# Kernel tuning notes

Hardware: AMD Instinct MI355X
Metric: run time of the kernel (lower is better)

## Reference

```python
import jax, jax.numpy as jnp
import numpy as np

TAU = 0.2
ALPHA = 0.8
EPS = 1e-8  # torch cosine_similarity eps
LAM_POS = 1.5  # generate_lambda()=0.5, +1 for extrapolation
LAM_NEG = 0.5  # interpolation lambda


def _cos_sim_matrix(x):
    # row-normalize with clamped norm (matches F.cosine_similarity eps), then gram matrix
    n = x / jnp.maximum(jnp.linalg.norm(x, axis=1, keepdims=True), EPS)
    return n @ n.T


def setup_inputs() -> dict:
    key = jax.random.key(0)
    N, D = 4096, 512
    emb = jax.random.normal(key, (N, D), dtype=jnp.float32)
    # SimCLR-style symmetric positive pairs: (2k,2k+1) and (2k+1,2k)
    base = np.arange(0, N, 2)
    fwd_pairs = np.stack([base, base + 1], axis=1)
    pairs = np.concatenate([fwd_pairs, fwd_pairs[:, ::-1]], axis=0)  # [N, 2]
    return {"embeddings": emb, "positive_pairs": jnp.asarray(pairs, dtype=jnp.int32)}


def reference(embeddings, positive_pairs):
    # stage == 'train' (quantile-thresholded hard-negative branch)
    N = embeddings.shape[0]
    ar = jnp.arange(N)
    pi, pj = positive_pairs[:, 0], positive_pairs[:, 1]
    # ordered positive mask (symmetric because pairs include both orientations)
    pos_mask = jnp.zeros((N, N), dtype=bool).at[pi, pj].set(True)

    # --- extrapolate positive pairs: row i -> 1.5*e_i - 0.5*e_j ---
    partner_pos = jnp.full((N,), -1, dtype=jnp.int32).at[pi].set(pj.astype(jnp.int32))
    in_pair = partner_pos >= 0
    pp = jnp.where(in_pair, partner_pos, 0)
    hard_pos_emb = jnp.where(
        in_pair[:, None],
        LAM_POS * embeddings - (LAM_POS - 1.0) * embeddings[pp],
        embeddings,
    )

    # --- interpolate negative pairs: row k -> 0.5*(e_k + e_partner) ---
    # Negative pairs are all ordered (i,j), i!=j, not positive, scattered in
    # row k is the largest i with (i,k) negative.
    valid = (~pos_mask.T) & (ar[None, :] != ar[:, None])  # valid[k, i] = (i,k) is negative
    partner_neg = jnp.max(jnp.where(valid, ar[None, :], -1), axis=1)
    hard_neg_emb = LAM_NEG * embeddings + (1.0 - LAM_NEG) * embeddings[partner_neg]

    # --- three NxN cosine-sim matrices, composed by the scatter pattern ---
    orig_sim = _cos_sim_matrix(embeddings)
    hard_pos_sim = _cos_sim_matrix(hard_pos_emb)
    hard_neg_sim = _cos_sim_matrix(hard_neg_emb)
    diag = jnp.eye(N, dtype=bool)
    sim = jnp.where(diag, orig_sim, jnp.where(pos_mask, hard_pos_sim, hard_neg_sim))

    # --- contrastive loss with per-row quantile hard-negative threshold ---
    mask = diag | pos_mask
    exp_sim = jnp.exp(sim / TAU)
    exp_masked = jnp.where(mask, 0.0, exp_sim)
    pos_sim = exp_sim[pi, pj]              # [P]
    exp_rows = exp_masked[pi]              # [P, N]
    thr = jnp.quantile(exp_rows, ALPHA, axis=1, keepdims=True)
    hard_neg_sum = jnp.sum(jnp.where(exp_rows >= thr, exp_rows, 0.0), axis=1)
    loss = -jnp.log(pos_sim / (pos_sim + hard_neg_sum))
    # torch sums loss_ij + loss_ji over all rows / (2*P); with symmetric pair
    # list this equals sum(loss_ij)/P
    return jnp.sum(loss) / positive_pairs.shape[0]
```

## Files before the change

kernel.cpp:

```cpp
#include <hip/hip_runtime.h>
#include <cmath>

#define DIM 512
#define TAU_INV 5.0f
#define EPSN 1e-8f
#define ALPHA_Q 0.8f
#define TPITCH 72

typedef __attribute__((ext_vector_type(8))) unsigned short us8;
typedef __attribute__((ext_vector_type(4))) unsigned short us4;
typedef __attribute__((ext_vector_type(8))) short s8v;
typedef __attribute__((ext_vector_type(4))) float f4;

__device__ __forceinline__ unsigned short f2h(float f) {
    _Float16 h = (_Float16)f;
    return *(const unsigned short*)&h;
}
__device__ __forceinline__ float h2f(unsigned u) {
    unsigned short us = (unsigned short)u;
    _Float16 h = *(const _Float16*)&us;
    return (float)h;
}
__device__ __forceinline__ unsigned key16(unsigned u) {
    return u ^ (0x8000u | (0x7FFFu & (0u - (u >> 15))));
}
__device__ __forceinline__ float keyval(unsigned k) {
    unsigned u = (k & 0x8000u) ? (k & 0x7FFFu) : ((~k) & 0xFFFFu);
    return h2f(u);
}

__global__ void k_scatter(const int* __restrict__ pairs, int* partner, int P) {
    int k = blockIdx.x * 256 + threadIdx.x;
    if (k < P) partner[pairs[2 * k]] = pairs[2 * k + 1];
}

__global__ __launch_bounds__(64) void k_prep(const float* __restrict__ emb,
                                             const int* __restrict__ partner,
                                             const int* __restrict__ pairs,
                                             unsigned short* __restrict__ mb,
                                             float* __restrict__ pos_term,
                                             int N, int P) {
    int bid = blockIdx.x, t = threadIdx.x;
    if (bid < N) {
        int i = bid;
        int q = N - 1;
        if (q == i || partner[q] == i) q = N - 2;
        if (q == i || partner[q] == i) q = N - 3;
        const float4* A = (const float4*)(emb + (size_t)i * DIM);
        const float4* B = (const float4*)(emb + (size_t)q * DIM);
        float4 a0 = A[t], a1 = A[t + 64];
        float4 b0 = B[t], b1 = B[t + 64];
        float h0x = 0.5f * (a0.x + b0.x), h0y = 0.5f * (a0.y + b0.y);
        float h0z = 0.5f * (a0.z + b0.z), h0w = 0.5f * (a0.w + b0.w);
        float h1x = 0.5f * (a1.x + b1.x), h1y = 0.5f * (a1.y + b1.y);
        float h1z = 0.5f * (a1.z + b1.z), h1w = 0.5f * (a1.w + b1.w);
        float ss = h0x * h0x + h0y * h0y + h0z * h0z + h0w * h0w
                 + h1x * h1x + h1y * h1y + h1z * h1z + h1w * h1w;
        for (int o = 32; o > 0; o >>= 1) ss += __shfl_xor(ss, o);
        float inv = 1.0f / fmaxf(sqrtf(ss), EPSN);
        us4 lo, hi;
        lo[0] = f2h(h0x * inv); lo[1] = f2h(h0y * inv);
        lo[2] = f2h(h0z * inv); lo[3] = f2h(h0w * inv);
        hi[0] = f2h(h1x * inv); hi[1] = f2h(h1y * inv);
        hi[2] = f2h(h1z * inv); hi[3] = f2h(h1w * inv);
        *(us4*)(mb + (size_t)i * DIM + t * 4) = lo;
        *(us4*)(mb + (size_t)i * DIM + 256 + t * 4) = hi;
    } else {
        int k = bid - N;
        int i = pairs[2 * k], j = pairs[2 * k + 1];
        const float4* A = (const float4*)(emb + (size_t)i * DIM);
        const float4* B = (const float4*)(emb + (size_t)j * DIM);
        float4 a0 = A[t], a1 = A[t + 64];
        float4 b0 = B[t], b1 = B[t + 64];
        float dab = 0.f, naa = 0.f, nbb = 0.f;
        float fa, fb;
        fa = 1.5f * a0.x - 0.5f * b0.x; fb = 1.5f * b0.x - 0.5f * a0.x; dab += fa * fb; naa += fa * fa; nbb += fb * fb;
        fa = 1.5f * a0.y - 0.5f * b0.y; fb = 1.5f * b0.y - 0.5f * a0.y; dab += fa * fb; naa += fa * fa; nbb += fb * fb;
        fa = 1.5f * a0.z - 0.5f * b0.z; fb = 1.5f * b0.z - 0.5f * a0.z; dab += fa * fb; naa += fa * fa; nbb += fb * fb;
        fa = 1.5f * a0.w - 0.5f * b0.w; fb = 1.5f * b0.w - 0.5f * a0.w; dab += fa * fb; naa += fa * fa; nbb += fb * fb;
        fa = 1.5f * a1.x - 0.5f * b1.x; fb = 1.5f * b1.x - 0.5f * a1.x; dab += fa * fb; naa += fa * fa; nbb += fb * fb;
        fa = 1.5f * a1.y - 0.5f * b1.y; fb = 1.5f * b1.y - 0.5f * a1.y; dab += fa * fb; naa += fa * fa; nbb += fb * fb;
        fa = 1.5f * a1.z - 0.5f * b1.z; fb = 1.5f * b1.z - 0.5f * a1.z; dab += fa * fb; naa += fa * fa; nbb += fb * fb;
        fa = 1.5f * a1.w - 0.5f * b1.w; fb = 1.5f * b1.w - 0.5f * a1.w; dab += fa * fb; naa += fa * fa; nbb += fb * fb;
        for (int o = 32; o > 0; o >>= 1) {
            dab += __shfl_xor(dab, o);
            naa += __shfl_xor(naa, o);
            nbb += __shfl_xor(nbb, o);
        }
        if (t == 0) {
            float sim = dab / (fmaxf(sqrtf(naa), EPSN) * fmaxf(sqrtf(nbb), EPSN));
            pos_term[k] = expf(sim * TAU_INV);
        }
    }
}

__global__ __launch_bounds__(256, 3) void k_gemm_sym(const unsigned short* __restrict__ mb,
                                                     unsigned short* __restrict__ S, int N) {
    __shared__ __align__(16) unsigned short smem[4 * 64 * TPITCH];
    int tid = threadIdx.x;
    int wave = tid >> 6, lane = tid & 63, quad = lane >> 4, l16 = lane & 15;
    int wr = (wave >> 1) * 64, wc = (wave & 1) * 64;

    int ntb = N >> 7;
    int bi = 0, rem = blockIdx.x, rowlen = ntb;
    while (rem >= rowlen) { rem -= rowlen; ++bi; --rowlen; }
    int bj = bi + rem;
    int iBase = bi * 128, jBase = bj * 128;
    int lrow = lane >> 2, lseg = lane & 3;

    const unsigned short* gA0 = mb + (size_t)(iBase + wave * 32 + lrow) * DIM + lseg * 8;
    const unsigned short* gA1 = gA0 + 16 * DIM;
    const unsigned short* gB0 = mb + (size_t)(jBase + wave * 32 + lrow) * DIM + lseg * 8;
    const unsigned short* gB1 = gB0 + 16 * DIM;

    __attribute__((address_space(3))) char* ldsBase =
        (__attribute__((address_space(3))) char*)smem;

#define STAGE(buf, koff)                                                                   \
    do {                                                                                   \
        __attribute__((address_space(3))) char* dA = ldsBase + (buf) * 16384 + wave * 2048;\
        __attribute__((address_space(3))) char* dB = dA + 8192;                            \
        __builtin_amdgcn_global_load_lds(                                                  \
            (const __attribute__((address_space(1))) void*)(gA0 + (koff)),                 \
            (__attribute__((address_space(3))) void*)(dA), 16, 0, 0);                      \
        __builtin_amdgcn_global_load_lds(                                                  \
            (const __attribute__((address_space(1))) void*)(gA1 + (koff)),                 \
            (__attribute__((address_space(3))) void*)(dA + 1024), 16, 0, 0);               \
        __builtin_amdgcn_global_load_lds(                                                  \
            (const __attribute__((address_space(1))) void*)(gB0 + (koff)),                 \
            (__attribute__((address_space(3))) void*)(dB), 16, 0, 0);                      \
        __builtin_amdgcn_global_load_lds(                                                  \
            (const __attribute__((address_space(1))) void*)(gB1 + (koff)),                 \
            (__attribute__((address_space(3))) void*)(dB + 1024), 16, 0, 0);               \
    } while (0)

    f4 acc[4][4];
    for (int i = 0; i < 4; ++i)
        for (int j = 0; j < 4; ++j) acc[i][j] = (f4){0.f, 0.f, 0.f, 0.f};

    STAGE(0, 0);
    __syncthreads();
    int cur = 0;
    for (int t = 0; t < 16; ++t) {
        if (t < 15) STAGE(cur ^ 1, (t + 1) * 32);
        const unsigned short* base = smem + cur * 8192;
        s8v a[4], b[4];
        #pragma unroll
        for (int i = 0; i < 4; ++i)
            a[i] = *(const s8v*)&base[(wr + i * 16 + l16) * 32 + quad * 8];
        #pragma unroll
        for (int j = 0; j < 4; ++j)
            b[j] = *(const s8v*)&base[4096 + (wc + j * 16 + l16) * 32 + quad * 8];
        #pragma unroll
        for (int i = 0; i < 4; ++i)
            #pragma unroll
            for (int j = 0; j < 4; ++j)
                acc[i][j] = __builtin_amdgcn_mfma_f32_16x16x32_f16(a[i], b[j], acc[i][j], 0, 0, 0);
        __syncthreads();
        cur ^= 1;
    }
#undef STAGE

    int rQ = iBase + wr + quad * 4;
    int cQ = jBase + wc + l16;
    for (int i = 0; i < 4; ++i)
        for (int j = 0; j < 4; ++j)
            for (int rr = 0; rr < 4; ++rr)
                S[(size_t)(rQ + i * 16 + rr) * N + cQ + j * 16] = f2h(acc[i][j][rr]);

    if (bi != bj) {
        unsigned short* T = smem + wave * 64 * TPITCH;
        #pragma unroll
        for (int i = 0; i < 4; ++i)
            #pragma unroll
            for (int j = 0; j < 4; ++j)
                #pragma unroll
                for (int rr = 0; rr < 4; ++rr) {
                    int tr = quad * 4 + i * 16 + rr;
                    int tc = l16 + j * 16;
                    T[tc * TPITCH + tr] = f2h(acc[i][j][rr]);
                }
        int lrow8 = lane >> 3, lseg8 = lane & 7;
        #pragma unroll
        for (int it = 0; it < 8; ++it) {
            int mr = it * 8 + lrow8;
            us8 v = *(const us8*)&T[mr * TPITCH + lseg8 * 8];
            *(us8*)&S[(size_t)(jBase + wc + mr) * N + iBase + wr + lseg8 * 8] = v;
        }
    }
}

__global__ __launch_bounds__(256) void k_gemm(const unsigned short* __restrict__ mb,
                                              unsigned short* __restrict__ S, int N, int rowBase) {
    __shared__ __align__(16) unsigned short As[128][32];
    __shared__ __align__(16) unsigned short Bs[128][32];
    int tid = threadIdx.x;
    int wave = tid >> 6, lane = tid & 63, quad = lane >> 4, l16 = lane & 15;
    int wr = (wave >> 1) * 64, wc = (wave & 1) * 64;
    int iBase = rowBase + blockIdx.y * 128;
    int jBase = blockIdx.x * 128;
    int lrow = lane >> 2, lseg = lane & 3;

    const unsigned short* gA0 = mb + (size_t)(iBase + wave * 32 + lrow) * DIM + lseg * 8;
    const unsigned short* gA1 = gA0 + 16 * DIM;
    const unsigned short* gB0 = mb + (size_t)(jBase + wave * 32 + lrow) * DIM + lseg * 8;
    const unsigned short* gB1 = gB0 + 16 * DIM;
    __attribute__((address_space(3))) char* ldsA =
        (__attribute__((address_space(3))) char*)As + wave * 2048;
    __attribute__((address_space(3))) char* ldsB =
        (__attribute__((address_space(3))) char*)Bs + wave * 2048;

    f4 acc[4][4];
    for (int i = 0; i < 4; ++i)
        for (int j = 0; j < 4; ++j) acc[i][j] = (f4){0.f, 0.f, 0.f, 0.f};

    for (int k0 = 0; k0 < DIM; k0 += 32) {
        __syncthreads();
        __builtin_amdgcn_global_load_lds(
            (const __attribute__((address_space(1))) void*)(gA0 + k0),
            (__attribute__((address_space(3))) void*)(ldsA), 16, 0, 0);
        __builtin_amdgcn_global_load_lds(
            (const __attribute__((address_space(1))) void*)(gA1 + k0),
            (__attribute__((address_space(3))) void*)(ldsA + 1024), 16, 0, 0);
        __builtin_amdgcn_global_load_lds(
            (const __attribute__((address_space(1))) void*)(gB0 + k0),
            (__attribute__((address_space(3))) void*)(ldsB), 16, 0, 0);
        __builtin_amdgcn_global_load_lds(
            (const __attribute__((address_space(1))) void*)(gB1 + k0),
            (__attribute__((address_space(3))) void*)(ldsB + 1024), 16, 0, 0);
        __syncthreads();

        s8v a[4], b[4];
        for (int i = 0; i < 4; ++i) a[i] = *(const s8v*)&As[wr + i * 16 + l16][quad * 8];
        for (int j = 0; j < 4; ++j) b[j] = *(const s8v*)&Bs[wc + j * 16 + l16][quad * 8];
        for (int i = 0; i < 4; ++i)
            for (int j = 0; j < 4; ++j)
                acc[i][j] = __builtin_amdgcn_mfma_f32_16x16x32_f16(a[i], b[j], acc[i][j], 0, 0, 0);
    }
    int rQ = blockIdx.y * 128 + wr + quad * 4;
    int cQ = jBase + wc + l16;
    for (int i = 0; i < 4; ++i)
        for (int j = 0; j < 4; ++j)
            for (int rr = 0; rr < 4; ++rr)
                S[(size_t)(rQ + i * 16 + rr) * N + cQ + j * 16] = f2h(acc[i][j][rr]);
}

__global__ __launch_bounds__(128, 4) void k_select(const unsigned short* __restrict__ Sb,
                                                   const int* __restrict__ pairs,
                                                   const float* __restrict__ pos_term,
                                                   float* __restrict__ losses,
                                                   int N, int r0, int r1, int P,
                                                   int klo, float frac) {
    int wid = threadIdx.x >> 6, lane = threadIdx.x & 63;
    int k = blockIdx.x * 2 + wid;
    if (k >= P) return;
    int row = pairs[2 * k];
    if (row < r0 || row >= r1) return;
    int pj = pairs[2 * k + 1];
    const us8* src8 = (const us8*)(Sb + (size_t)(row - r0) * N);

    unsigned kr[32];
    #pragma unroll
    for (int t = 0; t < 8; ++t)
        *(us8*)&kr[t * 4] = src8[t * 64 + lane];

    #pragma unroll
    for (int t = 0; t < 8; ++t) {
        int j0 = (t * 64 + lane) * 8;
        #pragma unroll
        for (int m = 0; m < 4; ++m) {
            unsigned p = kr[t * 4 + m];
            unsigned lo = key16(p & 0xFFFFu);
            unsigned hi = key16(p >> 16);
            int jlo = j0 + 2 * m, jhi = jlo + 1;
            if (jlo == row || jlo == pj) lo = 0u;
            if (jhi == row || jhi == pj) hi = 0u;
            kr[t * 4 + m] = lo | (hi << 16);
        }
    }

    int nmask = (pj == row) ? 1 : 2;
    int Nreal = N - nmask;
    int Rreal = klo - nmask;
    float pos = pos_term[k];
    float s = 0.f;

    if (Rreal < 0) {
        #pragma unroll
        for (int i = 0; i < 32; ++i) {
            unsigned lo = kr[i] & 0xFFFFu, hi = kr[i] >> 16;
            if (lo > 0u) s += __expf(keyval(lo) * TAU_INV);
            if (hi > 0u) s += __expf(keyval(hi) * TAU_INV);
        }
    } else {
        int lim = Nreal - Rreal - 1;
        unsigned lo_ = 16383u, hi_ = 49153u;
        while (lo_ < hi_) {
            unsigned mid = (lo_ + hi_) >> 1;
            unsigned cv = 0;
            #pragma unroll
            for (int i = 0; i < 32; ++i) {
                unsigned lo = kr[i] & 0xFFFFu, hi = kr[i] >> 16;
                cv += (unsigned)(lo > mid);
                cv += (unsigned)(hi > mid);
            }
            for (int o = 1; o < 64; o <<= 1) cv += (unsigned)__shfl_xor((int)cv, o);
            if (cv <= (unsigned)lim) hi_ = mid; else lo_ = mid + 1;
        }
        unsigned K1 = lo_;

        if (frac > 1e-9f) {
            unsigned cAv = 0, mymin = 0xFFFFFFFFu;
            #pragma unroll
            for (int i = 0; i < 32; ++i) {
                unsigned lo = kr[i] & 0xFFFFu, hi = kr[i] >> 16;
                bool glo = lo > K1, ghi = hi > K1;
                cAv += (unsigned)glo + (unsigned)ghi;
                if (glo && lo < mymin) mymin = lo;
                if (ghi && hi < mymin) mymin = hi;
            }
            for (int o = 1; o < 64; o <<= 1) {
                cAv += (unsigned)__shfl_xor((int)cAv, o);
                unsigned y = (unsigned)__shfl_xor((int)mymin, o);
                if (y < mymin) mymin = y;
            }
            unsigned cntAbove = cAv;
            unsigned K2;
            if (Rreal + 1 > Nreal - 1)                   K2 = K1;
            else if (Nreal - (int)cntAbove >= Rreal + 2) K2 = K1;
            else                                         K2 = mymin;
            float elo = __expf(keyval(K1) * TAU_INV);
            float ehi = __expf(keyval(K2) * TAU_INV);
            float thr = elo + frac * (ehi - elo);
            #pragma unroll
            for (int i = 0; i < 32; ++i) {
                unsigned lo = kr[i] & 0xFFFFu, hi = kr[i] >> 16;
                if (lo > 0u) { float ev = __expf(keyval(lo) * TAU_INV); if (ev >= thr) s += ev; }
                if (hi > 0u) { float ev = __expf(keyval(hi) * TAU_INV); if (ev >= thr) s += ev; }
            }
        } else {
            #pragma unroll
            for (int i = 0; i < 32; ++i) {
                unsigned lo = kr[i] & 0xFFFFu, hi = kr[i] >> 16;
                if (lo >= K1) s += __expf(keyval(lo) * TAU_INV);
                if (hi >= K1) s += __expf(keyval(hi) * TAU_INV);
            }
        }
    }

    for (int o = 1; o < 64; o <<= 1) s += __shfl_xor(s, o);
    if (lane == 0) losses[k] = logf((pos + s) / pos);
}

__global__ __launch_bounds__(256) void k_reduce(const float* __restrict__ losses,
                                                float* __restrict__ out, int P, float invP) {
    __shared__ float s_red[4];
    int tid = threadIdx.x, wid = tid >> 6, lane = tid & 63;
    float s = 0.f;
    for (int i = tid; i < P; i += 256) s += losses[i];
    for (int o = 1; o < 64; o <<= 1) s += __shfl_xor(s, o);
    if (lane == 0) s_red[wid] = s;
    __syncthreads();
    if (tid == 0) out[0] = (s_red[0] + s_red[1] + s_red[2] + s_red[3]) * invP;
}

extern "C" void kernel_launch(void* const* d_in, const int* in_sizes, int n_in,
                              void* d_out, int out_size, void* d_ws, size_t ws_size,
                              hipStream_t stream) {
    const float* emb = (const float*)d_in[0];
    const int* pairs = (const int*)d_in[1];
    float* out = (float*)d_out;
    int N = in_sizes[0] / DIM;
    int P = in_sizes[1] / 2;

    char* ws = (char*)d_ws;
    size_t off = 0;
    unsigned short* mb = (unsigned short*)(ws + off); off += (size_t)N * DIM * 2;
    int* partner = (int*)(ws + off);                  off += (size_t)N * 4;
    float* pos_term = (float*)(ws + off);             off += (size_t)P * 4;
    float* losses = (float*)(ws + off);               off += (size_t)P * 4;
    off = (off + 255) & ~(size_t)255;
    unsigned short* Sbuf = (unsigned short*)(ws + off);
    size_t avail = (ws_size > off) ? ws_size - off : 0;
    long maxRows = (long)(avail / ((size_t)N * 2));
    int chunk = (int)(maxRows - (maxRows % 128));
    if (chunk > N) chunk = N;
    if (chunk < 128) chunk = 128;

    k_scatter<<<dim3((P + 255) / 256), dim3(256), 0, stream>>>(pairs, partner, P);
    k_prep<<<dim3(N + P), dim3(64), 0, stream>>>(emb, partner, pairs, mb, pos_term, N, P);

    float qpos = ALPHA_Q * (float)(N - 1);
    int klo = (int)floorf(qpos);
    float frac = qpos - (float)klo;
    float invP = 1.0f / (float)P;

    if (chunk >= N) {
        int ntb = N >> 7;
        int nblk = ntb * (ntb + 1) / 2;
        k_gemm_sym<<<dim3(nblk), dim3(256), 0, stream>>>(mb, Sbuf, N);
        k_select<<<dim3((P + 1) / 2), dim3(128), 0, stream>>>(Sbuf, pairs, pos_term, losses,
                                                              N, 0, N, P, klo, frac);
    } else {
        for (int r0 = 0; r0 < N; r0 += chunk) {
            int rows = (N - r0 < chunk) ? (N - r0) : chunk;
            dim3 g(N / 128, rows / 128);
            k_gemm<<<g, dim3(256), 0, stream>>>(mb, Sbuf, N, r0);
            k_select<<<dim3((P + 1) / 2), dim3(128), 0, stream>>>(Sbuf, pairs, pos_term, losses,
                                                                  N, r0, r0 + rows, P, klo, frac);
        }
    }
    k_reduce<<<dim3(1), dim3(256), 0, stream>>>(losses, out, P, invP);
}
```

Before: 120.8 us.

## Split each selection row across two wavefronts with LDS-combined binary search

The quantile-selection kernel now assigns one row per 128-thread block, with each of the two wavefronts holding half the row (16 registers instead of 32). Per-iteration counts, the minimum above the threshold, and the final sums are combined through shared memory with block barriers. This halves per-thread register use and doubles the number of waves working on selection, aiming for higher occupancy and shorter per-row latency. The cost is a __syncthreads in every binary-search iteration plus the extra LDS traffic.

```diff
diff --git a/kernel.cpp b/kernel.cpp
--- a/kernel.cpp
+++ b/kernel.cpp
@@ -245,37 +245,40 @@
                 S[(size_t)(rQ + i * 16 + rr) * N + cQ + j * 16] = f2h(acc[i][j][rr]);
 }
 
-__global__ __launch_bounds__(128, 4) void k_select(const unsigned short* __restrict__ Sb,
+__global__ __launch_bounds__(128, 8) void k_select(const unsigned short* __restrict__ Sb,
                                                    const int* __restrict__ pairs,
                                                    const float* __restrict__ pos_term,
                                                    float* __restrict__ losses,
                                                    int N, int r0, int r1, int P,
                                                    int klo, float frac) {
+    __shared__ unsigned smc[20][2];
+    __shared__ unsigned smm[2];
+    __shared__ float    sf[2];
     int wid = threadIdx.x >> 6, lane = threadIdx.x & 63;
-    int k = blockIdx.x * 2 + wid;
+    int k = blockIdx.x;
     if (k >= P) return;
     int row = pairs[2 * k];
     if (row < r0 || row >= r1) return;
     int pj = pairs[2 * k + 1];
     const us8* src8 = (const us8*)(Sb + (size_t)(row - r0) * N);
 
-    unsigned kr[32];
+    unsigned kr[16];
     #pragma unroll
-    for (int t = 0; t < 8; ++t)
-        *(us8*)&kr[t * 4] = src8[t * 64 + lane];
+    for (int tt = 0; tt < 4; ++tt)
+        *(us8*)&kr[tt * 4] = src8[(wid * 4 + tt) * 64 + lane];
 
     #pragma unroll
-    for (int t = 0; t < 8; ++t) {
-        int j0 = (t * 64 + lane) * 8;
+    for (int tt = 0; tt < 4; ++tt) {
+        int j0 = ((wid * 4 + tt) * 64 + lane) * 8;
         #pragma unroll
         for (int m = 0; m < 4; ++m) {
-            unsigned p = kr[t * 4 + m];
+            unsigned p = kr[tt * 4 + m];
             unsigned lo = key16(p & 0xFFFFu);
             unsigned hi = key16(p >> 16);
             int jlo = j0 + 2 * m, jhi = jlo + 1;
             if (jlo == row || jlo == pj) lo = 0u;
             if (jhi == row || jhi == pj) hi = 0u;
-            kr[t * 4 + m] = lo | (hi << 16);
+            kr[tt * 4 + m] = lo | (hi << 16);
         }
     }
 
@@ -287,7 +290,7 @@
 
     if (Rreal < 0) {
         #pragma unroll
-        for (int i = 0; i < 32; ++i) {
+        for (int i = 0; i < 16; ++i) {
             unsigned lo = kr[i] & 0xFFFFu, hi = kr[i] >> 16;
             if (lo > 0u) s += __expf(keyval(lo) * TAU_INV);
             if (hi > 0u) s += __expf(keyval(hi) * TAU_INV);
@@ -295,24 +298,29 @@
     } else {
         int lim = Nreal - Rreal - 1;
         unsigned lo_ = 16383u, hi_ = 49153u;
+        int it = 0;
         while (lo_ < hi_) {
             unsigned mid = (lo_ + hi_) >> 1;
             unsigned cv = 0;
             #pragma unroll
-            for (int i = 0; i < 32; ++i) {
+            for (int i = 0; i < 16; ++i) {
                 unsigned lo = kr[i] & 0xFFFFu, hi = kr[i] >> 16;
                 cv += (unsigned)(lo > mid);
                 cv += (unsigned)(hi > mid);
             }
             for (int o = 1; o < 64; o <<= 1) cv += (unsigned)__shfl_xor((int)cv, o);
-            if (cv <= (unsigned)lim) hi_ = mid; else lo_ = mid + 1;
+            if (lane == 0) smc[it][wid] = cv;
+            __syncthreads();
+            unsigned cnt = smc[it][0] + smc[it][1];
+            if (cnt <= (unsigned)lim) hi_ = mid; else lo_ = mid + 1;
+            ++it;
         }
         unsigned K1 = lo_;
 
         if (frac > 1e-9f) {
             unsigned cAv = 0, mymin = 0xFFFFFFFFu;
             #pragma unroll
-            for (int i = 0; i < 32; ++i) {
+            for (int i = 0; i < 16; ++i) {
                 unsigned lo = kr[i] & 0xFFFFu, hi = kr[i] >> 16;
                 bool glo = lo > K1, ghi = hi > K1;
                 cAv += (unsigned)glo + (unsigned)ghi;
@@ -324,23 +332,26 @@
                 unsigned y = (unsigned)__shfl_xor((int)mymin, o);
                 if (y < mymin) mymin = y;
             }
-            unsigned cntAbove = cAv;
+            if (lane == 0) { smc[16][wid] = cAv; smm[wid] = mymin; }
+            __syncthreads();
+            unsigned cntAbove = smc[16][0] + smc[16][1];
+            unsigned mn = smm[0] < smm[1] ? smm[0] : smm[1];
             unsigned K2;
             if (Rreal + 1 > Nreal - 1)                   K2 = K1;
             else if (Nreal - (int)cntAbove >= Rreal + 2) K2 = K1;
-            else                                         K2 = mymin;
+            else                                         K2 = mn;
             float elo = __expf(keyval(K1) * TAU_INV);
             float ehi = __expf(keyval(K2) * TAU_INV);
             float thr = elo + frac * (ehi - elo);
             #pragma unroll
-            for (int i = 0; i < 32; ++i) {
+            for (int i = 0; i < 16; ++i) {
                 unsigned lo = kr[i] & 0xFFFFu, hi = kr[i] >> 16;
                 if (lo > 0u) { float ev = __expf(keyval(lo) * TAU_INV); if (ev >= thr) s += ev; }
                 if (hi > 0u) { float ev = __expf(keyval(hi) * TAU_INV); if (ev >= thr) s += ev; }
             }
         } else {
             #pragma unroll
-            for (int i = 0; i < 32; ++i) {
+            for (int i = 0; i < 16; ++i) {
                 unsigned lo = kr[i] & 0xFFFFu, hi = kr[i] >> 16;
                 if (lo >= K1) s += __expf(keyval(lo) * TAU_INV);
                 if (hi >= K1) s += __expf(keyval(hi) * TAU_INV);
@@ -349,7 +360,10 @@
     }
 
     for (int o = 1; o < 64; o <<= 1) s += __shfl_xor(s, o);
-    if (lane == 0) losses[k] = logf((pos + s) / pos);
+    if (lane == 0) sf[wid] = s;
+    __syncthreads();
+    if (threadIdx.x == 0)
+        losses[k] = logf((pos + sf[0] + sf[1]) / pos);
 }
 
 __global__ __launch_bounds__(256) void k_reduce(const float* __restrict__ losses,
@@ -399,15 +413,15 @@
         int ntb = N >> 7;
         int nblk = ntb * (ntb + 1) / 2;
         k_gemm_sym<<<dim3(nblk), dim3(256), 0, stream>>>(mb, Sbuf, N);
-        k_select<<<dim3((P + 1) / 2), dim3(128), 0, stream>>>(Sbuf, pairs, pos_term, losses,
-                                                              N, 0, N, P, klo, frac);
+        k_select<<<dim3(P), dim3(128), 0, stream>>>(Sbuf, pairs, pos_term, losses,
+                                                    N, 0, N, P, klo, frac);
     } else {
         for (int r0 = 0; r0 < N; r0 += chunk) {
             int rows = (N - r0 < chunk) ? (N - r0) : chunk;
             dim3 g(N / 128, rows / 128);
             k_gemm<<<g, dim3(256), 0, stream>>>(mb, Sbuf, N, r0);
-            k_select<<<dim3((P + 1) / 2), dim3(128), 0, stream>>>(Sbuf, pairs, pos_term, losses,
-                                                                  N, r0, r0 + rows, P, klo, frac);
+            k_select<<<dim3(P), dim3(128), 0, stream>>>(Sbuf, pairs, pos_term, losses,
+                                                        N, r0, r0 + rows, P, klo, frac);
         }
     }
     k_reduce<<<dim3(1), dim3(256), 0, stream>>>(losses, out, P, invP);
```

Measured after the change: 119.1 us, median of 3. Within noise of the previous version (-1.4%).
